# Kernel tuning notes

Measured on AMD Instinct MI355X. Metric: run time of the kernel, lower is better.

## Reference

```python
import jax, jax.numpy as jnp
import numpy as np

NB_HEAD = 16
SIZE_PER_HEAD = 64
D_MODEL = 1024
OUT_DIM = NB_HEAD * SIZE_PER_HEAD
BIG_NEG = 1e10


def setup_inputs() -> dict:
    key = jax.random.key(0)
    ks = jax.random.split(key, 6)
    B, L = 2, 2048
    q = jax.random.normal(ks[0], (B, L, D_MODEL), dtype=jnp.float32)
    k = jax.random.normal(ks[1], (B, L, D_MODEL), dtype=jnp.float32)
    v = jax.random.normal(ks[2], (B, L, D_MODEL), dtype=jnp.float32)
    v_mask = jnp.ones((B, L), dtype=jnp.float32)
    q_mask = jnp.ones((B, L), dtype=jnp.float32)
    # glorot_normal-ish init for the three projection kernels
    std = (2.0 / (D_MODEL + OUT_DIM)) ** 0.5
    q_kernel = jax.random.normal(ks[3], (D_MODEL, OUT_DIM), dtype=jnp.float32) * std
    k_kernel = jax.random.normal(ks[4], (D_MODEL, OUT_DIM), dtype=jnp.float32) * std
    v_kernel = jax.random.normal(ks[5], (D_MODEL, OUT_DIM), dtype=jnp.float32) * std
    return {"q": q, "k": k, "v": v, "v_mask": v_mask, "q_mask": q_mask,
            "q_kernel": q_kernel, "k_kernel": k_kernel, "v_kernel": v_kernel}


def reference(q, k, v, v_mask, q_mask, q_kernel, k_kernel, v_kernel):
    B, Lq, _ = q.shape
    Lk = k.shape[1]
    H, D = NB_HEAD, SIZE_PER_HEAD
    # projections -> [B, L, H, D]
    qw = (q @ q_kernel).reshape(B, Lq, H, D)
    kw = (k @ k_kernel).reshape(B, Lk, H, D)
    vw = (v @ v_kernel).reshape(B, Lk, H, D)
    # scaled dot-product scores [B, H, Lq, Lk]
    scores = jnp.einsum('bqhd,bkhd->bhqk', qw, kw) / jnp.sqrt(jnp.float32(D))
    # additive key mask (original permutes so mask broadcasts over key axis)
    scores = scores - (1.0 - v_mask)[:, None, None, :] * BIG_NEG
    a = jax.nn.softmax(scores, axis=-1)
    # weighted sum -> [B, Lq, H, D] -> [B, Lq, H*D]
    o = jnp.einsum('bhqk,bkhd->bqhd', a, vw).reshape(B, Lq, H * D)
    # multiplicative query mask on output
    o = o * q_mask[:, :, None]
    return o
```

## Files before the change

kernel.cpp:

```cpp
#include <hip/hip_runtime.h>
#include <hip/hip_bf16.h>

#define B_SZ 2
#define SEQ  2048
#define DM   1024
#define NH   16
#define HD   64

typedef __attribute__((ext_vector_type(8))) short bf16x8;
typedef __attribute__((ext_vector_type(4))) short bf16x4;
typedef __attribute__((ext_vector_type(4))) float f32x4;
typedef __attribute__((ext_vector_type(16))) float f32x16;
typedef unsigned long long ull;

__device__ __forceinline__ short f2b(float f) {
    __hip_bfloat16 h = __float2bfloat16(f);
    return *reinterpret_cast<short*>(&h);
}
__device__ __forceinline__ ull pack4(float a, float b, float c, float d) {
    union { bf16x4 v; ull u; } t;
    t.v[0] = f2b(a); t.v[1] = f2b(b); t.v[2] = f2b(c); t.v[3] = f2b(d);
    return t.u;
}

__device__ __forceinline__ void async_copy16(void* lds, const void* g) {
    __builtin_amdgcn_global_load_lds(
        (const __attribute__((address_space(1))) void*)g,
        (__attribute__((address_space(3))) void*)lds, 16, 0, 0);
}

__global__ __launch_bounds__(256) void kT(
    const float* __restrict__ w0, const float* __restrict__ w1, const float* __restrict__ w2,
    short* __restrict__ t0, short* __restrict__ t1, short* __restrict__ t2) {
    const float* w = blockIdx.z == 0 ? w0 : (blockIdx.z == 1 ? w1 : w2);
    short*       t = blockIdx.z == 0 ? t0 : (blockIdx.z == 1 ? t1 : t2);
    __shared__ float tile[64][65];
    int n0 = (blockIdx.x & 15) * 64, k0 = (blockIdx.x >> 4) * 64;
    int tid = threadIdx.x;
    int c = tid & 63, rr = tid >> 6;
#pragma unroll
    for (int i = 0; i < 16; i++) {
        int kk = i * 4 + rr;
        tile[kk][c] = w[(size_t)(k0 + kk) * DM + n0 + c];
    }
    __syncthreads();
#pragma unroll
    for (int i = 0; i < 16; i++) {
        int nn = i * 4 + rr;
        t[(size_t)(n0 + nn) * DM + k0 + c] = f2b(tile[c][nn]);
    }
}

__global__ __launch_bounds__(256) void kProj(
    const float* __restrict__ q, const float* __restrict__ k, const float* __restrict__ v,
    const short* __restrict__ wtq, const short* __restrict__ wtk, const short* __restrict__ wtv,
    short* __restrict__ qw, short* __restrict__ kw, short* __restrict__ vwT) {
    int z = blockIdx.z;
    const float* A  = z == 0 ? q : (z == 1 ? k : v);
    const short* Bt = z == 0 ? wtq : (z == 1 ? wtk : wtv);

    __shared__ short As[128 * 72];
    __shared__ short Bs[128 * 64];

    int tid = threadIdx.x;
    int m0 = blockIdx.y * 128, n0 = blockIdx.x * 128;
    int wv = tid >> 6, lane = tid & 63, quad = lane >> 4, ln = lane & 15;
    int rblk = (wv >> 1) * 64, cblk = (wv & 1) * 64;

    int rB = wv * 32;
    int srowB = rB + (lane >> 3), scolB = (lane & 7) * 8;
    int sr = tid >> 4, sc4 = (tid & 15) * 4;

    f32x4 zero = {0.f, 0.f, 0.f, 0.f};
    f32x4 acc[4][4];
#pragma unroll
    for (int rt = 0; rt < 4; rt++)
#pragma unroll
        for (int ct = 0; ct < 4; ct++) acc[rt][ct] = zero;

    for (int ks = 0; ks < DM; ks += 64) {
        const short* gB = Bt + (size_t)(n0 + srowB) * DM + ks + scolB;
#pragma unroll
        for (int i = 0; i < 4; i++)
            async_copy16(&Bs[(rB + i * 8) * 64], gB + (size_t)i * 8 * DM);
#pragma unroll
        for (int i = 0; i < 8; i++) {
            int row = i * 16 + sr;
            float4 av = *reinterpret_cast<const float4*>(
                &A[(size_t)(m0 + row) * DM + ks + sc4]);
            *reinterpret_cast<ull*>(&As[row * 72 + sc4]) =
                pack4(av.x, av.y, av.z, av.w);
        }
        __syncthreads();
#pragma unroll
        for (int kc = 0; kc < 2; kc++) {
            bf16x8 af[4], bfv[4];
#pragma unroll
            for (int rt = 0; rt < 4; rt++)
                af[rt] = *reinterpret_cast<bf16x8*>(&As[(rblk + rt * 16 + ln) * 72 + kc * 32 + quad * 8]);
#pragma unroll
            for (int ct = 0; ct < 4; ct++)
                bfv[ct] = *reinterpret_cast<bf16x8*>(&Bs[(cblk + ct * 16 + ln) * 64 + kc * 32 + quad * 8]);
#pragma unroll
            for (int rt = 0; rt < 4; rt++)
#pragma unroll
                for (int ct = 0; ct < 4; ct++)
                    acc[rt][ct] = __builtin_amdgcn_mfma_f32_16x16x32_bf16(
                        af[rt], bfv[ct], acc[rt][ct], 0, 0, 0);
        }
        __syncthreads();
    }

    if (z < 2) {
        short* C = z == 0 ? qw : kw;
#pragma unroll
        for (int rt = 0; rt < 4; rt++)
#pragma unroll
            for (int r = 0; r < 4; r++) {
                int row = m0 + rblk + rt * 16 + quad * 4 + r;
#pragma unroll
                for (int ct = 0; ct < 4; ct++)
                    C[(size_t)row * DM + n0 + cblk + ct * 16 + ln] = f2b(acc[rt][ct][r]);
            }
    } else {
#pragma unroll
        for (int rt = 0; rt < 4; rt++) {
            int srow0 = m0 + rblk + rt * 16 + quad * 4;
            int bb = srow0 >> 11, lk = srow0 & (SEQ - 1);
#pragma unroll
            for (int ct = 0; ct < 4; ct++) {
                int coln = n0 + cblk + ct * 16 + ln;
                int hh = coln >> 6, dd = coln & 63;
                *reinterpret_cast<ull*>(
                    &vwT[(((size_t)bb * NH + hh) * HD + dd) * SEQ + lk]) =
                    pack4(acc[rt][ct][0], acc[rt][ct][1], acc[rt][ct][2], acc[rt][ct][3]);
            }
        }
    }
}

__global__ __launch_bounds__(256, 2) void kAttn(
    const short* __restrict__ qw, const short* __restrict__ kw, const short* __restrict__ vwT,
    const float* __restrict__ vmask, const float* __restrict__ qmask, float* __restrict__ out) {
    int b = blockIdx.z, h = blockIdx.y, lq0 = blockIdx.x * 128;
    int tid = threadIdx.x, wv = tid >> 6, lane = tid & 63;
    int l5 = lane & 31, half = lane >> 5;

    __shared__ short Ks[128][72];
    __shared__ short Vt[64][136];

    const float C1 = 0.18033688f;
    const float MB = 1.4426950e10f;

    const short* qrow = qw + (size_t)(b * SEQ + lq0 + wv * 32 + l5) * DM + h * HD;
    bf16x8 qf[4];
#pragma unroll
    for (int ki = 0; ki < 4; ki++)
        qf[ki] = *reinterpret_cast<const bf16x8*>(qrow + ki * 16 + half * 8);

    float lrow = 0.f;
    f32x16 o0, o1;
#pragma unroll
    for (int i = 0; i < 16; i++) { o0[i] = 0.f; o1[i] = 0.f; }

    int krow = tid >> 1, kcol = (tid & 1) * 32;
    int vrow = tid >> 2, vcol = (tid & 3) * 32;
    const short* kp = kw + (size_t)(b * SEQ + krow) * DM + h * HD + kcol;
    const short* vp = vwT + ((size_t)(b * NH + h) * HD + vrow) * SEQ + vcol;
    const float* vmb = vmask + b * SEQ;

    bf16x8 kr[4], vr[4];
#pragma unroll
    for (int i = 0; i < 4; i++) {
        kr[i] = *reinterpret_cast<const bf16x8*>(kp + i * 8);
        vr[i] = *reinterpret_cast<const bf16x8*>(vp + i * 8);
    }

    for (int it = 0; it < SEQ / 128; it++) {
        int lk0 = it * 128;
#pragma unroll
        for (int i = 0; i < 4; i++) {
            *reinterpret_cast<bf16x8*>(&Ks[krow][kcol + i * 8]) = kr[i];
            *reinterpret_cast<bf16x8*>(&Vt[vrow][vcol + i * 8]) = vr[i];
        }
        __syncthreads();

        if (it + 1 < SEQ / 128) {
            kp += (size_t)128 * DM;
            vp += 128;
#pragma unroll
            for (int i = 0; i < 4; i++) {
                kr[i] = *reinterpret_cast<const bf16x8*>(kp + i * 8);
                vr[i] = *reinterpret_cast<const bf16x8*>(vp + i * 8);
            }
        }

        f32x16 s[4];
#pragma unroll
        for (int lt = 0; lt < 4; lt++)
#pragma unroll
            for (int i = 0; i < 16; i++) s[lt][i] = 0.f;
#pragma unroll
        for (int lt = 0; lt < 4; lt++)
#pragma unroll
            for (int ki = 0; ki < 4; ki++) {
                bf16x8 kf = *reinterpret_cast<bf16x8*>(&Ks[lt * 32 + l5][ki * 16 + half * 8]);
                s[lt] = __builtin_amdgcn_mfma_f32_32x32x16_bf16(kf, qf[ki], s[lt], 0, 0, 0);
            }

        float rs = 0.f;
        ull pk[4][4];
#pragma unroll
        for (int lt = 0; lt < 4; lt++)
#pragma unroll
            for (int g = 0; g < 4; g++) {
                float4 mv = *reinterpret_cast<const float4*>(
                    &vmb[lk0 + lt * 32 + 8 * g + 4 * half]);
                float p0 = exp2f(fmaf(s[lt][4 * g + 0], C1, (mv.x - 1.0f) * MB));
                float p1 = exp2f(fmaf(s[lt][4 * g + 1], C1, (mv.y - 1.0f) * MB));
                float p2 = exp2f(fmaf(s[lt][4 * g + 2], C1, (mv.z - 1.0f) * MB));
                float p3 = exp2f(fmaf(s[lt][4 * g + 3], C1, (mv.w - 1.0f) * MB));
                rs += (p0 + p1) + (p2 + p3);
                pk[lt][g] = pack4(p0, p1, p2, p3);
            }
        rs += __shfl_xor(rs, 32);
        lrow += rs;

#pragma unroll
        for (int ki = 0; ki < 8; ki++) {
            int lt = ki >> 1, mb = 2 * (ki & 1);
            ull mine = half ? pk[lt][mb + 1] : pk[lt][mb];
            ull send = half ? pk[lt][mb]     : pk[lt][mb + 1];
            ull rec  = __shfl_xor((long long)send, 32);
            union { ull u[2]; bf16x8 v; } fr;
            fr.u[0] = half ? rec : mine;
            fr.u[1] = half ? mine : rec;
            bf16x8 vf0 = *reinterpret_cast<bf16x8*>(&Vt[l5][ki * 16 + half * 8]);
            bf16x8 vf1 = *reinterpret_cast<bf16x8*>(&Vt[32 + l5][ki * 16 + half * 8]);
            o0 = __builtin_amdgcn_mfma_f32_32x32x16_bf16(vf0, fr.v, o0, 0, 0, 0);
            o1 = __builtin_amdgcn_mfma_f32_32x32x16_bf16(vf1, fr.v, o1, 0, 0, 0);
        }
        __syncthreads();
    }

    int lq = lq0 + wv * 32 + l5;
    float sc2 = (1.0f / lrow) * qmask[b * SEQ + lq];
    float* orow = out + (size_t)(b * SEQ + lq) * DM + h * HD;
#pragma unroll
    for (int g = 0; g < 4; g++) {
        float4 st0, st1;
        st0.x = o0[4 * g + 0] * sc2; st0.y = o0[4 * g + 1] * sc2;
        st0.z = o0[4 * g + 2] * sc2; st0.w = o0[4 * g + 3] * sc2;
        st1.x = o1[4 * g + 0] * sc2; st1.y = o1[4 * g + 1] * sc2;
        st1.z = o1[4 * g + 2] * sc2; st1.w = o1[4 * g + 3] * sc2;
        *reinterpret_cast<float4*>(&orow[8 * g + 4 * half]) = st0;
        *reinterpret_cast<float4*>(&orow[32 + 8 * g + 4 * half]) = st1;
    }
}

extern "C" void kernel_launch(void* const* d_in, const int* in_sizes, int n_in,
                              void* d_out, int out_size, void* d_ws, size_t ws_size,
                              hipStream_t stream) {
    const float* q  = (const float*)d_in[0];
    const float* k  = (const float*)d_in[1];
    const float* v  = (const float*)d_in[2];
    const float* vm = (const float*)d_in[3];
    const float* qm = (const float*)d_in[4];
    const float* qk = (const float*)d_in[5];
    const float* kk = (const float*)d_in[6];
    const float* vk = (const float*)d_in[7];
    float* out = (float*)d_out;

    short* ws  = (short*)d_ws;
    short* wtq = ws;
    short* wtk = wtq + 1024 * 1024;
    short* wtv = wtk + 1024 * 1024;
    short* qw  = wtv + 1024 * 1024;
    short* kw  = qw + (size_t)4096 * 1024;
    short* vwT = kw + (size_t)4096 * 1024;

    kT   <<<dim3(256, 1, 3), 256, 0, stream>>>(qk, kk, vk, wtq, wtk, wtv);
    kProj<<<dim3(8, 32, 3), 256, 0, stream>>>(q, k, v, wtq, wtk, wtv, qw, kw, vwT);
    kAttn<<<dim3(16, 16, 2), 256, 0, stream>>>(qw, kw, vwT, vm, qm, out);
}
```

Before: 240.6 us.

## Double-buffer K/V tiles in LDS and drop second barrier in attention loop

Result: slower. 267.3 us (+11.1%).

```diff
diff --git a/kernel.cpp b/kernel.cpp
--- a/kernel.cpp
+++ b/kernel.cpp
@@ -12,6 +12,7 @@
 typedef __attribute__((ext_vector_type(4))) float f32x4;
 typedef __attribute__((ext_vector_type(16))) float f32x16;
 typedef unsigned long long ull;
+typedef unsigned int u32;
 
 __device__ __forceinline__ short f2b(float f) {
     __hip_bfloat16 h = __float2bfloat16(f);
@@ -21,6 +22,11 @@
     union { bf16x4 v; ull u; } t;
     t.v[0] = f2b(a); t.v[1] = f2b(b); t.v[2] = f2b(c); t.v[3] = f2b(d);
     return t.u;
+}
+__device__ __forceinline__ ull pack4_trunc(float a, float b, float c, float d) {
+    u32 lo = (__float_as_uint(b) & 0xFFFF0000u) | (__float_as_uint(a) >> 16);
+    u32 hi = (__float_as_uint(d) & 0xFFFF0000u) | (__float_as_uint(c) >> 16);
+    return ((ull)hi << 32) | lo;
 }
 
 __device__ __forceinline__ void async_copy16(void* lds, const void* g) {
@@ -146,8 +152,8 @@
     int tid = threadIdx.x, wv = tid >> 6, lane = tid & 63;
     int l5 = lane & 31, half = lane >> 5;
 
-    __shared__ short Ks[128][72];
-    __shared__ short Vt[64][136];
+    __shared__ short Ks[2][128][72];
+    __shared__ short Vt[2][64][136];
 
     const float C1 = 0.18033688f;
     const float MB = 1.4426950e10f;
@@ -159,9 +165,9 @@
         qf[ki] = *reinterpret_cast<const bf16x8*>(qrow + ki * 16 + half * 8);
 
     float lrow = 0.f;
-    f32x16 o0, o1;
-#pragma unroll
-    for (int i = 0; i < 16; i++) { o0[i] = 0.f; o1[i] = 0.f; }
+    f32x16 o0, o1, Z;
+#pragma unroll
+    for (int i = 0; i < 16; i++) { o0[i] = 0.f; o1[i] = 0.f; Z[i] = 0.f; }
 
     int krow = tid >> 1, kcol = (tid & 1) * 32;
     int vrow = tid >> 2, vcol = (tid & 3) * 32;
@@ -175,14 +181,15 @@
         kr[i] = *reinterpret_cast<const bf16x8*>(kp + i * 8);
         vr[i] = *reinterpret_cast<const bf16x8*>(vp + i * 8);
     }
+#pragma unroll
+    for (int i = 0; i < 4; i++) {
+        *reinterpret_cast<bf16x8*>(&Ks[0][krow][kcol + i * 8]) = kr[i];
+        *reinterpret_cast<bf16x8*>(&Vt[0][vrow][vcol + i * 8]) = vr[i];
+    }
 
     for (int it = 0; it < SEQ / 128; it++) {
+        int cur = it & 1;
         int lk0 = it * 128;
-#pragma unroll
-        for (int i = 0; i < 4; i++) {
-            *reinterpret_cast<bf16x8*>(&Ks[krow][kcol + i * 8]) = kr[i];
-            *reinterpret_cast<bf16x8*>(&Vt[vrow][vcol + i * 8]) = vr[i];
-        }
         __syncthreads();
 
         if (it + 1 < SEQ / 128) {
@@ -197,16 +204,15 @@
 
         f32x16 s[4];
 #pragma unroll
-        for (int lt = 0; lt < 4; lt++)
-#pragma unroll
-            for (int i = 0; i < 16; i++) s[lt][i] = 0.f;
-#pragma unroll
-        for (int lt = 0; lt < 4; lt++)
-#pragma unroll
-            for (int ki = 0; ki < 4; ki++) {
-                bf16x8 kf = *reinterpret_cast<bf16x8*>(&Ks[lt * 32 + l5][ki * 16 + half * 8]);
+        for (int lt = 0; lt < 4; lt++) {
+            bf16x8 kf = *reinterpret_cast<bf16x8*>(&Ks[cur][lt * 32 + l5][half * 8]);
+            s[lt] = __builtin_amdgcn_mfma_f32_32x32x16_bf16(kf, qf[0], Z, 0, 0, 0);
+#pragma unroll
+            for (int ki = 1; ki < 4; ki++) {
+                kf = *reinterpret_cast<bf16x8*>(&Ks[cur][lt * 32 + l5][ki * 16 + half * 8]);
                 s[lt] = __builtin_amdgcn_mfma_f32_32x32x16_bf16(kf, qf[ki], s[lt], 0, 0, 0);
             }
+        }
 
         float rs = 0.f;
         ull pk[4][4];
@@ -221,7 +227,7 @@
                 float p2 = exp2f(fmaf(s[lt][4 * g + 2], C1, (mv.z - 1.0f) * MB));
                 float p3 = exp2f(fmaf(s[lt][4 * g + 3], C1, (mv.w - 1.0f) * MB));
                 rs += (p0 + p1) + (p2 + p3);
-                pk[lt][g] = pack4(p0, p1, p2, p3);
+                pk[lt][g] = pack4_trunc(p0, p1, p2, p3);
             }
         rs += __shfl_xor(rs, 32);
         lrow += rs;
@@ -235,12 +241,20 @@
             union { ull u[2]; bf16x8 v; } fr;
             fr.u[0] = half ? rec : mine;
             fr.u[1] = half ? mine : rec;
-            bf16x8 vf0 = *reinterpret_cast<bf16x8*>(&Vt[l5][ki * 16 + half * 8]);
-            bf16x8 vf1 = *reinterpret_cast<bf16x8*>(&Vt[32 + l5][ki * 16 + half * 8]);
+            bf16x8 vf0 = *reinterpret_cast<bf16x8*>(&Vt[cur][l5][ki * 16 + half * 8]);
+            bf16x8 vf1 = *reinterpret_cast<bf16x8*>(&Vt[cur][32 + l5][ki * 16 + half * 8]);
             o0 = __builtin_amdgcn_mfma_f32_32x32x16_bf16(vf0, fr.v, o0, 0, 0, 0);
             o1 = __builtin_amdgcn_mfma_f32_32x32x16_bf16(vf1, fr.v, o1, 0, 0, 0);
         }
-        __syncthreads();
+
+        if (it + 1 < SEQ / 128) {
+            int nxt = cur ^ 1;
+#pragma unroll
+            for (int i = 0; i < 4; i++) {
+                *reinterpret_cast<bf16x8*>(&Ks[nxt][krow][kcol + i * 8]) = kr[i];
+                *reinterpret_cast<bf16x8*>(&Vt[nxt][vrow][vcol + i * 8]) = vr[i];
+            }
+        }
     }
 
     int lq = lq0 + wv * 32 + l5;
```

## Route softmax probabilities through LDS and use cheaper bf16 packing

Applied to the files above, without the earlier changes.

Result: slower. 249.9 us (+3.9%).

```diff
diff --git a/kernel.cpp b/kernel.cpp
--- a/kernel.cpp
+++ b/kernel.cpp
@@ -12,15 +12,24 @@
 typedef __attribute__((ext_vector_type(4))) float f32x4;
 typedef __attribute__((ext_vector_type(16))) float f32x16;
 typedef unsigned long long ull;
+typedef unsigned int u32;
 
 __device__ __forceinline__ short f2b(float f) {
     __hip_bfloat16 h = __float2bfloat16(f);
     return *reinterpret_cast<short*>(&h);
 }
-__device__ __forceinline__ ull pack4(float a, float b, float c, float d) {
-    union { bf16x4 v; ull u; } t;
-    t.v[0] = f2b(a); t.v[1] = f2b(b); t.v[2] = f2b(c); t.v[3] = f2b(d);
+__device__ __forceinline__ ull pack4_rn(float a, float b, float c, float d) {
+    union { __hip_bfloat162 h[2]; ull u; } t;
+    float2 lo; lo.x = a; lo.y = b;
+    float2 hi; hi.x = c; hi.y = d;
+    t.h[0] = __float22bfloat162_rn(lo);
+    t.h[1] = __float22bfloat162_rn(hi);
     return t.u;
+}
+__device__ __forceinline__ ull pack4_trunc(float a, float b, float c, float d) {
+    u32 lo = (__float_as_uint(b) & 0xFFFF0000u) | (__float_as_uint(a) >> 16);
+    u32 hi = (__float_as_uint(d) & 0xFFFF0000u) | (__float_as_uint(c) >> 16);
+    return ((ull)hi << 32) | lo;
 }
 
 __device__ __forceinline__ void async_copy16(void* lds, const void* g) {
@@ -89,7 +98,7 @@
             float4 av = *reinterpret_cast<const float4*>(
                 &A[(size_t)(m0 + row) * DM + ks + sc4]);
             *reinterpret_cast<ull*>(&As[row * 72 + sc4]) =
-                pack4(av.x, av.y, av.z, av.w);
+                pack4_rn(av.x, av.y, av.z, av.w);
         }
         __syncthreads();
 #pragma unroll
@@ -133,7 +142,7 @@
                 int hh = coln >> 6, dd = coln & 63;
                 *reinterpret_cast<ull*>(
                     &vwT[(((size_t)bb * NH + hh) * HD + dd) * SEQ + lk]) =
-                    pack4(acc[rt][ct][0], acc[rt][ct][1], acc[rt][ct][2], acc[rt][ct][3]);
+                    pack4_rn(acc[rt][ct][0], acc[rt][ct][1], acc[rt][ct][2], acc[rt][ct][3]);
             }
         }
     }
@@ -148,6 +157,7 @@
 
     __shared__ short Ks[128][72];
     __shared__ short Vt[64][136];
+    __shared__ short Ps[4][32][136];
 
     const float C1 = 0.18033688f;
     const float MB = 1.4426950e10f;
@@ -209,7 +219,6 @@
             }
 
         float rs = 0.f;
-        ull pk[4][4];
 #pragma unroll
         for (int lt = 0; lt < 4; lt++)
 #pragma unroll
@@ -221,24 +230,23 @@
                 float p2 = exp2f(fmaf(s[lt][4 * g + 2], C1, (mv.z - 1.0f) * MB));
                 float p3 = exp2f(fmaf(s[lt][4 * g + 3], C1, (mv.w - 1.0f) * MB));
                 rs += (p0 + p1) + (p2 + p3);
-                pk[lt][g] = pack4(p0, p1, p2, p3);
+                *reinterpret_cast<ull*>(&Ps[wv][l5][lt * 32 + 8 * g + 4 * half]) =
+                    pack4_trunc(p0, p1, p2, p3);
             }
         rs += __shfl_xor(rs, 32);
         lrow += rs;
 
+        bf16x8 pf[8];
+#pragma unroll
+        for (int ki = 0; ki < 8; ki++)
+            pf[ki] = *reinterpret_cast<bf16x8*>(&Ps[wv][l5][ki * 16 + half * 8]);
+
 #pragma unroll
         for (int ki = 0; ki < 8; ki++) {
-            int lt = ki >> 1, mb = 2 * (ki & 1);
-            ull mine = half ? pk[lt][mb + 1] : pk[lt][mb];
-            ull send = half ? pk[lt][mb]     : pk[lt][mb + 1];
-            ull rec  = __shfl_xor((long long)send, 32);
-            union { ull u[2]; bf16x8 v; } fr;
-            fr.u[0] = half ? rec : mine;
-            fr.u[1] = half ? mine : rec;
             bf16x8 vf0 = *reinterpret_cast<bf16x8*>(&Vt[l5][ki * 16 + half * 8]);
             bf16x8 vf1 = *reinterpret_cast<bf16x8*>(&Vt[32 + l5][ki * 16 + half * 8]);
-            o0 = __builtin_amdgcn_mfma_f32_32x32x16_bf16(vf0, fr.v, o0, 0, 0, 0);
-            o1 = __builtin_amdgcn_mfma_f32_32x32x16_bf16(vf1, fr.v, o1, 0, 0, 0);
+            o0 = __builtin_amdgcn_mfma_f32_32x32x16_bf16(vf0, pf[ki], o0, 0, 0, 0);
+            o1 = __builtin_amdgcn_mfma_f32_32x32x16_bf16(vf1, pf[ki], o1, 0, 0, 0);
         }
         __syncthreads();
     }
```
